# Kernel optimization log

Measured on AMD Instinct MI355X. Metric: run time of the kernel, lower is better.

The kernel has to match this reference:

```python
import jax, jax.numpy as jnp
import numpy as np

DIM = 768
NUM_HEADS = 8
HEAD_DIM = DIM // NUM_HEADS


def setup_inputs() -> dict:
    key = jax.random.key(0)
    ks = jax.random.split(key, 5)
    B, N, C = 16, 4096, DIM
    x = jax.random.normal(ks[0], (B, N, C), dtype=jnp.float32)
    # nn.Linear(dim, dim*3): weight [3C, C], bias [3C]
    w_qkv = jax.random.normal(ks[1], (3 * C, C), dtype=jnp.float32) * (C ** -0.5)
    b_qkv = jax.random.normal(ks[2], (3 * C,), dtype=jnp.float32) * 0.02
    w_proj = jax.random.normal(ks[3], (C, C), dtype=jnp.float32) * (C ** -0.5)
    b_proj = jax.random.normal(ks[4], (C,), dtype=jnp.float32) * 0.02
    return {"x": x, "w_qkv": w_qkv, "b_qkv": b_qkv, "w_proj": w_proj, "b_proj": b_proj}


def reference(x, w_qkv, b_qkv, w_proj, b_proj):
    B, N, C = x.shape
    H, D = NUM_HEADS, C // NUM_HEADS
    # qkv projection: [B,N,3C] -> [3,B,H,N,D]
    qkv = x @ w_qkv.T + b_qkv
    qkv = qkv.reshape(B, N, 3, H, D).transpose(2, 0, 3, 1, 4)
    q, k, v = qkv[0], qkv[1], qkv[2]
    # dynamic_scale=True: scale by N^-0.5
    q = q * (N ** -0.5)
    # channel attention: contract over tokens N -> [B,H,D,D]
    attn = jnp.einsum("bhnd,bhne->bhde", q, k)
    attn = jax.nn.softmax(attn, axis=-1)
    # (attn @ v^T)^T -> [B,H,N,D]
    out = jnp.einsum("bhde,bhne->bhnd", attn, v)
    out = out.transpose(0, 2, 1, 3).reshape(B, N, C)
    return out @ w_proj.T + b_proj
```

## Files before the change

### kernel.cpp

```cpp
#include <hip/hip_runtime.h>
#include <hip/hip_bf16.h>
#include <stdint.h>

typedef __bf16 bf16;
typedef __bf16 bf16x8 __attribute__((ext_vector_type(8)));
typedef __bf16 bf16x4 __attribute__((ext_vector_type(4)));
typedef float f32x4 __attribute__((ext_vector_type(4)));

__device__ __forceinline__ void gl_lds16(const bf16* g, bf16* l) {
  __builtin_amdgcn_global_load_lds(
      (const __attribute__((address_space(1))) void*)g,
      (__attribute__((address_space(3))) void*)l, 16, 0, 0);
}

__global__ void cvt_f32_bf16(const float* __restrict__ in, bf16* __restrict__ out, int n4) {
  int i = blockIdx.x * blockDim.x + threadIdx.x;
  if (i < n4) {
    float4 v = ((const float4*)in)[i];
    bf16x4 o;
    o[0] = (bf16)v.x; o[1] = (bf16)v.y; o[2] = (bf16)v.z; o[3] = (bf16)v.w;
    ((bf16x4*)out)[i] = o;
  }
}

template<int EPI>
__global__ __launch_bounds__(256) void gemm_bt(
    const bf16* __restrict__ A, const bf16* __restrict__ B,
    const float* __restrict__ bias, void* __restrict__ C0, void* __restrict__ C1,
    void* __restrict__ C2, int M, int N, int K, int nbn)
{
  __shared__ __align__(16) bf16 sA[128 * 32];
  __shared__ __align__(16) bf16 sB[128 * 32];
  int tiles = gridDim.x;
  int bid = blockIdx.x;
  int tile = ((bid & 7) * (tiles >> 3)) + (bid >> 3);
  int bm = tile / nbn, bn = tile % nbn;
  int m0 = bm * 128, n0 = bn * 128;
  int t = threadIdx.x;
  int wave = t >> 6, lane = t & 63;
  int wm = wave >> 1, wn = wave & 1;
  int l16 = lane & 15, quad = lane >> 4;

  f32x4 acc[4][4] = {};

  int rA = (wave * 2) * 16 + (lane >> 2);
  int kk = (lane & 3) * 8;
  const bf16* gA = A + (long)(m0 + rA) * K + kk;
  const bf16* gB = B + (long)(n0 + rA) * K + kk;

  for (int k0 = 0; k0 < K; k0 += 32) {
    gl_lds16(gA + k0,          &sA[(wave * 2) * 512]);
    gl_lds16(gA + 16 * K + k0, &sA[(wave * 2 + 1) * 512]);
    gl_lds16(gB + k0,          &sB[(wave * 2) * 512]);
    gl_lds16(gB + 16 * K + k0, &sB[(wave * 2 + 1) * 512]);
    __syncthreads();
    bf16x8 af[4], bfr[4];
#pragma unroll
    for (int mi = 0; mi < 4; mi++)
      af[mi] = *(const bf16x8*)&sA[(wm * 64 + mi * 16 + l16) * 32 + quad * 8];
#pragma unroll
    for (int ni = 0; ni < 4; ni++)
      bfr[ni] = *(const bf16x8*)&sB[(wn * 64 + ni * 16 + l16) * 32 + quad * 8];
#pragma unroll
    for (int mi = 0; mi < 4; mi++)
#pragma unroll
      for (int ni = 0; ni < 4; ni++)
        acc[mi][ni] = __builtin_amdgcn_mfma_f32_16x16x32_bf16(af[mi], bfr[ni], acc[mi][ni], 0, 0, 0);
    __syncthreads();
  }

  if (EPI == 1) {
#pragma unroll
    for (int mi = 0; mi < 4; mi++) {
      int row = m0 + wm * 64 + mi * 16 + quad * 4;
#pragma unroll
      for (int ni = 0; ni < 4; ni++) {
        int col = n0 + wn * 64 + ni * 16 + l16;
        float bv = bias[col];
#pragma unroll
        for (int r = 0; r < 4; r++)
          ((float*)C0)[(long)(row + r) * N + col] = acc[mi][ni][r] + bv;
      }
    }
  } else if (n0 < 1536) {
    bf16* T = (n0 < 768) ? (bf16*)C0 : (bf16*)C1;
    int coff = (n0 < 768) ? 0 : 768;
    float scale = (n0 < 768) ? 0.015625f : 1.0f;
    int b = m0 >> 12;
    int tokB = m0 & 4095;
#pragma unroll
    for (int mi = 0; mi < 4; mi++) {
      int tokN = tokB + wm * 64 + mi * 16 + quad * 4;
#pragma unroll
      for (int ni = 0; ni < 4; ni++) {
        int col = n0 + wn * 64 + ni * 16 + l16;
        float bv = bias[col];
        bf16x4 o;
#pragma unroll
        for (int r = 0; r < 4; r++) o[r] = (bf16)((acc[mi][ni][r] + bv) * scale);
        *(bf16x4*)&T[((long)(b * 768 + (col - coff))) * 4096 + tokN] = o;
      }
    }
  } else {
    bf16* V = (bf16*)C2;
#pragma unroll
    for (int mi = 0; mi < 4; mi++) {
      int row = m0 + wm * 64 + mi * 16 + quad * 4;
#pragma unroll
      for (int ni = 0; ni < 4; ni++) {
        int col = n0 + wn * 64 + ni * 16 + l16;
        float bv = bias[col];
#pragma unroll
        for (int r = 0; r < 4; r++)
          V[(long)(row + r) * 768 + (col - 1536)] = (bf16)(acc[mi][ni][r] + bv);
      }
    }
  }
}

__global__ __launch_bounds__(256) void attn_qk(
    const bf16* __restrict__ qT, const bf16* __restrict__ kT, float* __restrict__ part)
{
  __shared__ __align__(16) bf16 sQ[96 * 32];
  __shared__ __align__(16) bf16 sK[96 * 32];
  int bid = blockIdx.x;
  int bh = bid >> 3, s = bid & 7;
  int b = bh >> 3, h = bh & 7;
  int t = threadIdx.x;
  int wave = t >> 6, lane = t & 63;
  int wm = wave >> 1, wn = wave & 1;
  int l16 = lane & 15, quad = lane >> 4;
  f32x4 acc[3][3] = {};
  const bf16* Qb = qT + ((long)(b * 768 + h * 96)) * 4096 + s * 512;
  const bf16* Kb = kT + ((long)(b * 768 + h * 96)) * 4096 + s * 512;

  int rowc = lane >> 2;
  int ko = (lane & 3) * 8;

  for (int it = 0; it < 16; it++) {
#pragma unroll
    for (int j = 0; j < 3; j++) {
      int c2 = wave * 3 + j;
      int c = (c2 < 6) ? c2 : c2 - 6;
      int row = c * 16 + rowc;
      const bf16* src = ((c2 < 6) ? Qb : Kb) + (long)row * 4096 + it * 32 + ko;
      bf16* dst = ((c2 < 6) ? sQ : sK) + c * 512;
      gl_lds16(src, dst);
    }
    __syncthreads();
    bf16x8 af[3], bfr[3];
#pragma unroll
    for (int mi = 0; mi < 3; mi++)
      af[mi] = *(const bf16x8*)&sQ[(wm * 48 + mi * 16 + l16) * 32 + quad * 8];
#pragma unroll
    for (int ni = 0; ni < 3; ni++)
      bfr[ni] = *(const bf16x8*)&sK[(wn * 48 + ni * 16 + l16) * 32 + quad * 8];
#pragma unroll
    for (int mi = 0; mi < 3; mi++)
#pragma unroll
      for (int ni = 0; ni < 3; ni++)
        acc[mi][ni] = __builtin_amdgcn_mfma_f32_16x16x32_bf16(af[mi], bfr[ni], acc[mi][ni], 0, 0, 0);
    __syncthreads();
  }
  float* pout = part + (long)bid * 9216;
#pragma unroll
  for (int mi = 0; mi < 3; mi++)
#pragma unroll
    for (int ni = 0; ni < 3; ni++) {
      int row = wm * 48 + mi * 16 + quad * 4;
      int col = wn * 48 + ni * 16 + l16;
#pragma unroll
      for (int r = 0; r < 4; r++)
        pout[(row + r) * 96 + col] = acc[mi][ni][r];
    }
}

__global__ __launch_bounds__(256) void softmax_attn(const float* __restrict__ part, bf16* __restrict__ attn)
{
  __shared__ float s[96 * 97];
  int bh = blockIdx.x;
  int t = threadIdx.x;
  const float* p0 = part + (long)bh * 8 * 9216;
  for (int e = t; e < 9216; e += 256) {
    float v = 0.f;
#pragma unroll
    for (int k = 0; k < 8; k++) v += p0[k * 9216 + e];
    int r = e / 96, c = e % 96;
    s[r * 97 + c] = v;
  }
  __syncthreads();
  if (t < 96) {
    float m = -1e30f;
    for (int i = 0; i < 96; i++) m = fmaxf(m, s[t * 97 + i]);
    float sum = 0.f;
    for (int i = 0; i < 96; i++) {
      float ev = __expf(s[t * 97 + i] - m);
      s[t * 97 + i] = ev;
      sum += ev;
    }
    float inv = 1.f / sum;
    bf16* ao = attn + (long)bh * 9216 + t * 96;
    for (int i = 0; i < 96; i++) ao[i] = (bf16)(s[t * 97 + i] * inv);
  }
}

__global__ __launch_bounds__(256) void attn_v(
    const bf16* __restrict__ V, const bf16* __restrict__ attn, bf16* __restrict__ out2)
{
  __shared__ __align__(16) bf16 sV[128 * 96];
  __shared__ __align__(16) bf16 sAt[96 * 96];
  int bh = blockIdx.x >> 5, tb = blockIdx.x & 31;
  int b = bh >> 3, h = bh & 7;
  int tok0 = tb * 128;
  int t = threadIdx.x;
  int wave = t >> 6, lane = t & 63;
  int wm = wave >> 1, wn = wave & 1;
  int l16 = lane & 15, quad = lane >> 4;
  f32x4 acc[4][3] = {};
  const bf16* Vb = V + (long)b * 4096 * 768 + h * 96;

#pragma unroll
  for (int j = 0; j < 6; j++) {
    int c = wave * 6 + j;
    int g = c * 64 + lane;
    int tok = g / 12, cc = g % 12;
    gl_lds16(Vb + (long)(tok0 + tok) * 768 + cc * 8, &sV[c * 512]);
  }
  for (int c = wave; c < 18; c += 4) {
    int g = c * 64 + lane;
    int d = g / 12, cc = g % 12;
    gl_lds16(attn + (long)bh * 9216 + d * 96 + cc * 8, &sAt[c * 512]);
  }
  __syncthreads();
#pragma unroll
  for (int ks = 0; ks < 3; ks++) {
    bf16x8 af[4], bfr[3];
#pragma unroll
    for (int mi = 0; mi < 4; mi++)
      af[mi] = *(const bf16x8*)&sV[(wm * 64 + mi * 16 + l16) * 96 + ks * 32 + quad * 8];
#pragma unroll
    for (int ni = 0; ni < 3; ni++)
      bfr[ni] = *(const bf16x8*)&sAt[(wn * 48 + ni * 16 + l16) * 96 + ks * 32 + quad * 8];
#pragma unroll
    for (int mi = 0; mi < 4; mi++)
#pragma unroll
      for (int ni = 0; ni < 3; ni++)
        acc[mi][ni] = __builtin_amdgcn_mfma_f32_16x16x32_bf16(af[mi], bfr[ni], acc[mi][ni], 0, 0, 0);
  }
  bf16* ob = out2 + (long)(b * 4096 + tok0) * 768 + h * 96;
#pragma unroll
  for (int mi = 0; mi < 4; mi++)
#pragma unroll
    for (int ni = 0; ni < 3; ni++) {
      int row = wm * 64 + mi * 16 + quad * 4;
      int col = wn * 48 + ni * 16 + l16;
#pragma unroll
      for (int r = 0; r < 4; r++)
        ob[(long)(row + r) * 768 + col] = (bf16)acc[mi][ni][r];
    }
}

extern "C" void kernel_launch(void* const* d_in, const int* in_sizes, int n_in,
                              void* d_out, int out_size, void* d_ws, size_t ws_size,
                              hipStream_t stream) {
  const float* x      = (const float*)d_in[0];
  const float* w_qkv  = (const float*)d_in[1];
  const float* b_qkv  = (const float*)d_in[2];
  const float* w_proj = (const float*)d_in[3];
  const float* b_proj = (const float*)d_in[4];

  char* ws = (char*)d_ws;
  bf16*  Xb     = (bf16*)ws;
  float* part   = (float*)ws;
  bf16*  out2   = (bf16*)ws;
  bf16*  Wqkvb  = (bf16*)(ws + 100663296);
  bf16*  Wprojb = (bf16*)(ws + 104202240);
  bf16*  qT     = (bf16*)(ws + 105381888);
  bf16*  kT     = (bf16*)(ws + 206045184);
  bf16*  Vbuf   = (bf16*)(ws + 306708480);
  bf16*  attnb  = (bf16*)(ws + 407371776);

  cvt_f32_bf16<<<(12582912 + 255) / 256, 256, 0, stream>>>(x, Xb, 12582912);
  cvt_f32_bf16<<<(442368 + 255) / 256, 256, 0, stream>>>(w_qkv, Wqkvb, 442368);
  cvt_f32_bf16<<<(147456 + 255) / 256, 256, 0, stream>>>(w_proj, Wprojb, 147456);

  gemm_bt<0><<<512 * 18, 256, 0, stream>>>(Xb, Wqkvb, b_qkv, qT, kT, Vbuf, 65536, 2304, 768, 18);
  attn_qk<<<1024, 256, 0, stream>>>(qT, kT, part);
  softmax_attn<<<128, 256, 0, stream>>>(part, attnb);
  attn_v<<<4096, 256, 0, stream>>>(Vbuf, attnb, out2);
  gemm_bt<1><<<512 * 6, 256, 0, stream>>>(out2, Wprojb, b_proj, d_out, nullptr, nullptr, 65536, 768, 768, 6);
}
```

Measured before the change: 981.5 us.

## Split QKV GEMM, swap MFMA operands for transposed stores, swizzle attn_qk LDS, wave-per-row softmax

The QKV GEMM is split into two launches: a Q/K launch with swapped MFMA operands so accumulator lanes map to tokens for the transposed store, and a separate V launch with a plain row-major bf16 epilogue. Launch bounds now request 6 waves per SIMD. attn_qk loads 64-wide K chunks into XOR-swizzled LDS to cut bank conflicts and halve barrier iterations. Softmax changes from one thread per row in one block per head to one wavefront per row with shuffle reductions, which greatly raises parallelism. The Q/K stores become scalar 2-byte writes, which may coalesce less well than the previous bf16x4 stores.

```diff
diff --git a/kernel.cpp b/kernel.cpp
--- a/kernel.cpp
+++ b/kernel.cpp
@@ -24,10 +24,10 @@
 }
 
 template<int EPI>
-__global__ __launch_bounds__(256) void gemm_bt(
+__global__ __launch_bounds__(256, 6) void gemm_bt(
     const bf16* __restrict__ A, const bf16* __restrict__ B,
     const float* __restrict__ bias, void* __restrict__ C0, void* __restrict__ C1,
-    void* __restrict__ C2, int M, int N, int K, int nbn)
+    int M, int N, int K, int nbn)
 {
   __shared__ __align__(16) bf16 sA[128 * 32];
   __shared__ __align__(16) bf16 sB[128 * 32];
@@ -64,12 +64,37 @@
 #pragma unroll
     for (int mi = 0; mi < 4; mi++)
 #pragma unroll
-      for (int ni = 0; ni < 4; ni++)
-        acc[mi][ni] = __builtin_amdgcn_mfma_f32_16x16x32_bf16(af[mi], bfr[ni], acc[mi][ni], 0, 0, 0);
-    __syncthreads();
-  }
-
-  if (EPI == 1) {
+      for (int ni = 0; ni < 4; ni++) {
+        if (EPI == 0)
+          acc[mi][ni] = __builtin_amdgcn_mfma_f32_16x16x32_bf16(bfr[ni], af[mi], acc[mi][ni], 0, 0, 0);
+        else
+          acc[mi][ni] = __builtin_amdgcn_mfma_f32_16x16x32_bf16(af[mi], bfr[ni], acc[mi][ni], 0, 0, 0);
+      }
+    __syncthreads();
+  }
+
+  if (EPI == 0) {
+    bf16* T;
+    int coff;
+    float scale;
+    if (n0 < 768) { T = (bf16*)C0; coff = 0;   scale = 0.015625f; }
+    else          { T = (bf16*)C1; coff = 768; scale = 1.0f; }
+    int b = m0 >> 12, tokB = m0 & 4095;
+#pragma unroll
+    for (int ni = 0; ni < 4; ni++) {
+      int ch = n0 + wn * 64 + ni * 16 + quad * 4;
+      float4 bv = *(const float4*)&bias[ch];
+#pragma unroll
+      for (int mi = 0; mi < 4; mi++) {
+        int tok = tokB + wm * 64 + mi * 16 + l16;
+        long base = ((long)(b * 768 + ch - coff)) * 4096 + tok;
+        T[base]         = (bf16)((acc[mi][ni][0] + bv.x) * scale);
+        T[base + 4096]  = (bf16)((acc[mi][ni][1] + bv.y) * scale);
+        T[base + 8192]  = (bf16)((acc[mi][ni][2] + bv.z) * scale);
+        T[base + 12288] = (bf16)((acc[mi][ni][3] + bv.w) * scale);
+      }
+    }
+  } else {
 #pragma unroll
     for (int mi = 0; mi < 4; mi++) {
       int row = m0 + wm * 64 + mi * 16 + quad * 4;
@@ -78,41 +103,11 @@
         int col = n0 + wn * 64 + ni * 16 + l16;
         float bv = bias[col];
 #pragma unroll
-        for (int r = 0; r < 4; r++)
-          ((float*)C0)[(long)(row + r) * N + col] = acc[mi][ni][r] + bv;
-      }
-    }
-  } else if (n0 < 1536) {
-    bf16* T = (n0 < 768) ? (bf16*)C0 : (bf16*)C1;
-    int coff = (n0 < 768) ? 0 : 768;
-    float scale = (n0 < 768) ? 0.015625f : 1.0f;
-    int b = m0 >> 12;
-    int tokB = m0 & 4095;
-#pragma unroll
-    for (int mi = 0; mi < 4; mi++) {
-      int tokN = tokB + wm * 64 + mi * 16 + quad * 4;
-#pragma unroll
-      for (int ni = 0; ni < 4; ni++) {
-        int col = n0 + wn * 64 + ni * 16 + l16;
-        float bv = bias[col];
-        bf16x4 o;
-#pragma unroll
-        for (int r = 0; r < 4; r++) o[r] = (bf16)((acc[mi][ni][r] + bv) * scale);
-        *(bf16x4*)&T[((long)(b * 768 + (col - coff))) * 4096 + tokN] = o;
-      }
-    }
-  } else {
-    bf16* V = (bf16*)C2;
-#pragma unroll
-    for (int mi = 0; mi < 4; mi++) {
-      int row = m0 + wm * 64 + mi * 16 + quad * 4;
-#pragma unroll
-      for (int ni = 0; ni < 4; ni++) {
-        int col = n0 + wn * 64 + ni * 16 + l16;
-        float bv = bias[col];
-#pragma unroll
-        for (int r = 0; r < 4; r++)
-          V[(long)(row + r) * 768 + (col - 1536)] = (bf16)(acc[mi][ni][r] + bv);
+        for (int r = 0; r < 4; r++) {
+          float v = acc[mi][ni][r] + bv;
+          if (EPI == 1) ((float*)C0)[(long)(row + r) * N + col] = v;
+          else          ((bf16*)C0)[(long)(row + r) * N + col] = (bf16)v;
+        }
       }
     }
   }
@@ -121,10 +116,11 @@
 __global__ __launch_bounds__(256) void attn_qk(
     const bf16* __restrict__ qT, const bf16* __restrict__ kT, float* __restrict__ part)
 {
-  __shared__ __align__(16) bf16 sQ[96 * 32];
-  __shared__ __align__(16) bf16 sK[96 * 32];
+  __shared__ __align__(16) bf16 sQ[96 * 64];
+  __shared__ __align__(16) bf16 sK[96 * 64];
   int bid = blockIdx.x;
-  int bh = bid >> 3, s = bid & 7;
+  int bh = bid >> 3, s = bid & 3 | ((bid >> 2) & 1) << 2;
+  s = bid & 7;
   int b = bh >> 3, h = bh & 7;
   int t = threadIdx.x;
   int wave = t >> 6, lane = t & 63;
@@ -134,32 +130,38 @@
   const bf16* Qb = qT + ((long)(b * 768 + h * 96)) * 4096 + s * 512;
   const bf16* Kb = kT + ((long)(b * 768 + h * 96)) * 4096 + s * 512;
 
-  int rowc = lane >> 2;
-  int ko = (lane & 3) * 8;
-
-  for (int it = 0; it < 16; it++) {
-#pragma unroll
-    for (int j = 0; j < 3; j++) {
-      int c2 = wave * 3 + j;
-      int c = (c2 < 6) ? c2 : c2 - 6;
-      int row = c * 16 + rowc;
-      const bf16* src = ((c2 < 6) ? Qb : Kb) + (long)row * 4096 + it * 32 + ko;
-      bf16* dst = ((c2 < 6) ? sQ : sK) + c * 512;
+  int rsub = lane >> 3;
+  int ksw = ((lane & 7) ^ (lane >> 3)) * 8;
+
+  for (int it = 0; it < 8; it++) {
+#pragma unroll
+    for (int j = 0; j < 6; j++) {
+      int c2 = wave * 6 + j;
+      int c = (c2 < 12) ? c2 : c2 - 12;
+      const bf16* src = ((c2 < 12) ? Qb : Kb) + (long)(c * 8 + rsub) * 4096 + it * 64 + ksw;
+      bf16* dst = ((c2 < 12) ? sQ : sK) + c * 512;
       gl_lds16(src, dst);
     }
     __syncthreads();
-    bf16x8 af[3], bfr[3];
-#pragma unroll
-    for (int mi = 0; mi < 3; mi++)
-      af[mi] = *(const bf16x8*)&sQ[(wm * 48 + mi * 16 + l16) * 32 + quad * 8];
-#pragma unroll
-    for (int ni = 0; ni < 3; ni++)
-      bfr[ni] = *(const bf16x8*)&sK[(wn * 48 + ni * 16 + l16) * 32 + quad * 8];
-#pragma unroll
-    for (int mi = 0; mi < 3; mi++)
-#pragma unroll
-      for (int ni = 0; ni < 3; ni++)
-        acc[mi][ni] = __builtin_amdgcn_mfma_f32_16x16x32_bf16(af[mi], bfr[ni], acc[mi][ni], 0, 0, 0);
+#pragma unroll
+    for (int ks = 0; ks < 2; ks++) {
+      bf16x8 af[3], bfr[3];
+#pragma unroll
+      for (int mi = 0; mi < 3; mi++) {
+        int R = wm * 48 + mi * 16 + l16;
+        af[mi] = *(const bf16x8*)&sQ[R * 64 + (((ks * 4 + quad) ^ (l16 & 7)) * 8)];
+      }
+#pragma unroll
+      for (int ni = 0; ni < 3; ni++) {
+        int R = wn * 48 + ni * 16 + l16;
+        bfr[ni] = *(const bf16x8*)&sK[R * 64 + (((ks * 4 + quad) ^ (l16 & 7)) * 8)];
+      }
+#pragma unroll
+      for (int mi = 0; mi < 3; mi++)
+#pragma unroll
+        for (int ni = 0; ni < 3; ni++)
+          acc[mi][ni] = __builtin_amdgcn_mfma_f32_16x16x32_bf16(af[mi], bfr[ni], acc[mi][ni], 0, 0, 0);
+    }
     __syncthreads();
   }
   float* pout = part + (long)bid * 9216;
@@ -177,31 +179,28 @@
 
 __global__ __launch_bounds__(256) void softmax_attn(const float* __restrict__ part, bf16* __restrict__ attn)
 {
-  __shared__ float s[96 * 97];
-  int bh = blockIdx.x;
-  int t = threadIdx.x;
-  const float* p0 = part + (long)bh * 8 * 9216;
-  for (int e = t; e < 9216; e += 256) {
-    float v = 0.f;
-#pragma unroll
-    for (int k = 0; k < 8; k++) v += p0[k * 9216 + e];
-    int r = e / 96, c = e % 96;
-    s[r * 97 + c] = v;
-  }
-  __syncthreads();
-  if (t < 96) {
-    float m = -1e30f;
-    for (int i = 0; i < 96; i++) m = fmaxf(m, s[t * 97 + i]);
-    float sum = 0.f;
-    for (int i = 0; i < 96; i++) {
-      float ev = __expf(s[t * 97 + i] - m);
-      s[t * 97 + i] = ev;
-      sum += ev;
-    }
-    float inv = 1.f / sum;
-    bf16* ao = attn + (long)bh * 9216 + t * 96;
-    for (int i = 0; i < 96; i++) ao[i] = (bf16)(s[t * 97 + i] * inv);
-  }
+  int row = blockIdx.x * 4 + (threadIdx.x >> 6);
+  int lane = threadIdx.x & 63;
+  int bh = row / 96, d = row - bh * 96;
+  const float* p = part + (long)bh * 8 * 9216 + d * 96;
+  float va = 0.f, vb = 0.f;
+#pragma unroll
+  for (int k = 0; k < 8; k++) {
+    va += p[k * 9216 + lane];
+    if (lane < 32) vb += p[k * 9216 + 64 + lane];
+  }
+  float m = (lane < 32) ? fmaxf(va, vb) : va;
+#pragma unroll
+  for (int sft = 32; sft; sft >>= 1) m = fmaxf(m, __shfl_xor(m, sft));
+  float ea = __expf(va - m);
+  float eb = (lane < 32) ? __expf(vb - m) : 0.f;
+  float s2 = ea + eb;
+#pragma unroll
+  for (int sft = 32; sft; sft >>= 1) s2 += __shfl_xor(s2, sft);
+  float inv = 1.f / s2;
+  bf16* ao = attn + (long)bh * 9216 + d * 96;
+  ao[lane] = (bf16)(ea * inv);
+  if (lane < 32) ao[64 + lane] = (bf16)(eb * inv);
 }
 
 __global__ __launch_bounds__(256) void attn_v(
@@ -284,9 +283,10 @@
   cvt_f32_bf16<<<(442368 + 255) / 256, 256, 0, stream>>>(w_qkv, Wqkvb, 442368);
   cvt_f32_bf16<<<(147456 + 255) / 256, 256, 0, stream>>>(w_proj, Wprojb, 147456);
 
-  gemm_bt<0><<<512 * 18, 256, 0, stream>>>(Xb, Wqkvb, b_qkv, qT, kT, Vbuf, 65536, 2304, 768, 18);
+  gemm_bt<0><<<512 * 12, 256, 0, stream>>>(Xb, Wqkvb, b_qkv, qT, kT, 65536, 4096, 768, 12);
+  gemm_bt<2><<<512 * 6, 256, 0, stream>>>(Xb, Wqkvb + 1536 * 768, b_qkv + 1536, Vbuf, nullptr, 65536, 768, 768, 6);
   attn_qk<<<1024, 256, 0, stream>>>(qT, kT, part);
-  softmax_attn<<<128, 256, 0, stream>>>(part, attnb);
+  softmax_attn<<<3072, 256, 0, stream>>>(part, attnb);
   attn_v<<<4096, 256, 0, stream>>>(Vbuf, attnb, out2);
-  gemm_bt<1><<<512 * 6, 256, 0, stream>>>(out2, Wprojb, b_proj, d_out, nullptr, nullptr, 65536, 768, 768, 6);
-}
+  gemm_bt<1><<<512 * 6, 256, 0, stream>>>(out2, Wprojb, b_proj, d_out, nullptr, 65536, 768, 768, 6);
+}
```

New measurement: 2.237 ms. +128.0%, slower.
